# Optimization experiments

Hardware: AMD Instinct MI355X
Metric: run time of the kernel (lower is better)

The kernel has to match this reference:

```python
import jax, jax.numpy as jnp
import numpy as np

B = 8192
D_IN, D1, D2, D3, D_OUT = 784, 256, 1024, 256, 10
N_STEPS = 20
LR_INFER = 0.1
GAMMA = 0.1


def setup_inputs() -> dict:
    key = jax.random.key(0)
    ks = jax.random.split(key, 17)
    inp = {
        "x": jax.random.normal(ks[0], (B, D_IN), dtype=jnp.float32),
        # state inits (original does randn*0.1 inside forward)
        "x1_0": jax.random.normal(ks[1], (B, D1), dtype=jnp.float32) * 0.1,
        "x2_0": jax.random.normal(ks[2], (B, D2), dtype=jnp.float32) * 0.1,
        "x3_0": jax.random.normal(ks[3], (B, D3), dtype=jnp.float32) * 0.1,
        "x4_0": jax.random.normal(ks[4], (B, D_OUT), dtype=jnp.float32) * 0.1,
        # parameters (randn*0.1 per __init__)
        "W1": jax.random.normal(ks[5], (D_IN, D1), dtype=jnp.float32) * 0.1,
        "W2": jax.random.normal(ks[6], (D1, D2), dtype=jnp.float32) * 0.1,
        "W3": jax.random.normal(ks[7], (D2, D3), dtype=jnp.float32) * 0.1,
        "W4": jax.random.normal(ks[8], (D3, D_OUT), dtype=jnp.float32) * 0.1,
        "b1": jnp.zeros((D1,), dtype=jnp.float32),
        "b2": jnp.zeros((D2,), dtype=jnp.float32),
        "b3": jnp.zeros((D3,), dtype=jnp.float32),
        "b4": jnp.zeros((D_OUT,), dtype=jnp.float32),
        "L1": jax.random.normal(ks[9], (D1, D1), dtype=jnp.float32) * 0.1,
        "L2": jax.random.normal(ks[10], (D2, D2), dtype=jnp.float32) * 0.1,
        "L3": jax.random.normal(ks[11], (D3, D3), dtype=jnp.float32) * 0.1,
    }
    return inp


def reference(x, x1_0, x2_0, x3_0, x4_0, W1, W2, W3, W4, b1, b2, b3, b4, L1, L2, L3):
    sig = jax.nn.sigmoid
    # x1_pred depends only on the (constant) input x; compute once.
    x1_pred = sig(x @ W1 + b1)  # [B, D1]

    def step(carry, _):
        x1, x2, x3 = carry
        x3_pred = sig(x2 @ W3 + b3)        # [B, D3]
        x2_pred = sig(x1 @ W2 + b2)        # [B, D2]
        x4_pred = x3 @ W4 + b4             # [B, D_OUT]
        eps4 = x4_pred - x4_0
        eps3 = x3_pred - x3
        eps2 = x2_pred - x2
        eps1 = x1_pred - x1
        x3_grad = -eps3 + eps4 @ W4.T - GAMMA * (x3 @ L3)
        x2_grad = -eps2 + eps3 @ W3.T - GAMMA * (x2 @ L2)
        x1_grad = -eps1 + eps2 @ W2.T - GAMMA * (x1 @ L1)
        return (x1 - LR_INFER * x1_grad,
                x2 - LR_INFER * x2_grad,
                x3 - LR_INFER * x3_grad), None

    (x1, x2, x3), _ = jax.lax.scan(step, (x1_0, x2_0, x3_0), None, length=N_STEPS)
    return x3 @ W4 + b4  # [B, D_OUT]
```

## Files before the change

### kernel.cpp

```cpp
#include <hip/hip_runtime.h>
#include <hip/hip_bf16.h>
#include <cstdint>
#include <cstring>


#define LRC 0.1f

typedef unsigned short u16;
typedef unsigned int u32;
typedef __attribute__((ext_vector_type(4))) float f32x4;
typedef __attribute__((ext_vector_type(8))) __bf16 bf16x8;

__device__ __forceinline__ u16 f2b(float v) {
  __hip_bfloat16 h = __float2bfloat16(v);
  union { __hip_bfloat16 h; u16 u; } c; c.h = h; return c.u;
}
__device__ __forceinline__ float b2f(u16 u) {
  union { u16 u; __hip_bfloat16 h; } c; c.u = u; return __bfloat162float(c.h);
}
__device__ __forceinline__ float sigf(float x) { return 1.0f / (1.0f + expf(-x)); }

__device__ __forceinline__ void gll16(const void* g, void* l) {
  __builtin_amdgcn_global_load_lds((const __attribute__((address_space(1))) u32*)g,
                                   (__attribute__((address_space(3))) u32*)l,
                                   16, 0, 0);
}

struct GemmDesc {
  const u16* A; const u16* Bt;
  const u16* A2; const u16* Bt2;
  const float* bias; const float* master; const float* pred; const float* aux;
  const u16* eprev;
  float* outF; u16* outB;
  int lda, ldb, lda2, ldb2, K, K2, N, tnl, nblocks, epi;
};
struct Descs { GemmDesc d[6]; int nd; };

__global__ __launch_bounds__(256) void k_gemm_multi(Descs P) {
  int bid = blockIdx.x;
  int base = 0, di = 0;
  while (di + 1 < P.nd && bid >= base + P.d[di].nblocks) { base += P.d[di].nblocks; ++di; }
  const GemmDesc& d = P.d[di];
  int t = bid - base;
  int tid = threadIdx.x;

  if (d.epi == 5) {
    int i = t * 256 + tid;
    int m = i / 10, n = i - m * 10;
    if (m < 8192) {
      const float* xr = d.master + (size_t)m * 256;
      float acc = 0.f;
      #pragma unroll 4
      for (int k = 0; k < 256; ++k) acc = fmaf(xr[k], d.pred[k * 10 + n], acc);
      d.outB[(size_t)m * 32 + n] = f2b(acc + d.bias[n] - d.aux[i]);
    }
    return;
  }

  __shared__ u16 ldsA[8192];
  __shared__ u16 ldsB[8192];

  int w = tid >> 6, l = tid & 63;
  int wm = w & 1, wn = w >> 1;
  int lrow = l & 15, kgrp = l >> 4;

  int tnl = d.tnl;
  int j = t >> 3;
  int tm = (t & 7) * (d.nblocks >> (3 + tnl)) + (j >> tnl);
  int tnn = j & ((1 << tnl) - 1);
  int m0 = tm * 128, n0 = tnn * 128;

  f32x4 zero = {0.f, 0.f, 0.f, 0.f};
  f32x4 acc[4][4];
  #pragma unroll
  for (int a = 0; a < 4; ++a)
    #pragma unroll
    for (int b = 0; b < 4; ++b) acc[a][b] = zero;

  int srow = l >> 2;
  int scol = (l & 3) * 8;

  auto run = [&](const u16* A, int lda, const u16* Bt, int ldb, int K) {
    for (int k0 = 0; k0 < K;) {
      int nsub = (K - k0 >= 64) ? 2 : 1;
      for (int i = 0; i < 2 * nsub; ++i) {
        int c = i * 4 + w;
        int ks = c >> 3, rb = c & 7;
        int row = rb * 16 + srow;
        int col = k0 + ks * 32 + scol;
        gll16(A  + (size_t)(m0 + row) * lda + col, &ldsA[c * 512]);
        gll16(Bt + (size_t)(n0 + row) * ldb + col, &ldsB[c * 512]);
      }
      __syncthreads();
      for (int ks = 0; ks < nsub; ++ks) {
        bf16x8 af[4], bfr[4];
        #pragma unroll
        for (int mi = 0; mi < 4; ++mi)
          af[mi] = *(const bf16x8*)&ldsA[ks * 4096 + (wm * 64 + mi * 16 + lrow) * 32 + kgrp * 8];
        #pragma unroll
        for (int ni = 0; ni < 4; ++ni)
          bfr[ni] = *(const bf16x8*)&ldsB[ks * 4096 + (wn * 64 + ni * 16 + lrow) * 32 + kgrp * 8];
        #pragma unroll
        for (int mi = 0; mi < 4; ++mi)
          #pragma unroll
          for (int ni = 0; ni < 4; ++ni)
            acc[mi][ni] = __builtin_amdgcn_mfma_f32_16x16x32_bf16(af[mi], bfr[ni], acc[mi][ni], 0, 0, 0);
      }
      __syncthreads();
      k0 += nsub * 32;
    }
  };

  run(d.A, d.lda, d.Bt, d.ldb, d.K);
  if (d.K2 > 0) run(d.A2, d.lda2, d.Bt2, d.ldb2, d.K2);

  int epi = d.epi;
  #pragma unroll
  for (int mi = 0; mi < 4; ++mi) {
    #pragma unroll
    for (int ni = 0; ni < 4; ++ni) {
      #pragma unroll
      for (int j2 = 0; j2 < 4; ++j2) {
        int row = m0 + wm * 64 + mi * 16 + kgrp * 4 + j2;
        int col = n0 + wn * 64 + ni * 16 + lrow;
        size_t idx = (size_t)row * d.N + col;
        float a = acc[mi][ni][j2];
        if (epi == 1) {
          float s = sigf(a + d.bias[col]);
          d.outB[idx] = f2b(s - d.master[idx]);
        } else if (epi == 2) {
          d.outF[idx] = sigf(a + d.bias[col]);
        } else if (epi == 3) {
          float v = d.outF[idx];
          float nv = v + LRC * (d.pred[idx] - v) - LRC * a;
          d.outF[idx] = nv; d.outB[idx] = f2b(nv);
        } else {
          float v = d.outF[idx];
          float nv = v + LRC * b2f(d.eprev[idx]) - LRC * a;
          d.outF[idx] = nv; d.outB[idx] = f2b(nv);
        }
      }
    }
  }
}

__global__ void k_state_init(const float* __restrict__ src, float* __restrict__ dstF,
                             u16* __restrict__ dstB, int n) {
  int i = blockIdx.x * 256 + threadIdx.x;
  if (i < n) { float v = src[i]; dstF[i] = v; dstB[i] = f2b(v); }
}
__global__ void k_transpose_scale(const float* __restrict__ src, u16* __restrict__ dst,
                                  int R, int C, float scale) {
  int i = blockIdx.x * 256 + threadIdx.x;
  if (i < R * C) { int r = i / C, c = i - r * C; dst[c * R + r] = f2b(scale * src[i]); }
}
__global__ void k_conv_bf(const float* __restrict__ src, u16* __restrict__ dst, int n) {
  int i = blockIdx.x * 256 + threadIdx.x;
  if (i < n) dst[i] = f2b(src[i]);
}
__global__ void k_w4pad(const float* __restrict__ W4, u16* __restrict__ dst) {
  int i = blockIdx.x * 256 + threadIdx.x;
  if (i < 256 * 32) { int n = i >> 5, k = i & 31; dst[i] = (k < 10) ? f2b(W4[n * 10 + k]) : (u16)0; }
}
__global__ void k_zero16(u16* __restrict__ dst, int n) {
  int i = blockIdx.x * 256 + threadIdx.x;
  if (i < n) dst[i] = 0;
}
__global__ void k_xsplit(const float* __restrict__ x, u16* __restrict__ dst) {
  int i = blockIdx.x * 256 + threadIdx.x;
  if (i < 8192 * 1600) {
    int m = i / 1600, c = i - m * 1600;
    u16 o = 0;
    if (c < 784) o = f2b(x[m * 784 + c]);
    else if (c >= 800 && c < 1584) {
      float v = x[m * 784 + (c - 800)];
      float h = b2f(f2b(v));
      o = f2b(v - h);
    }
    dst[i] = o;
  }
}
__global__ void k_w1c(const float* __restrict__ W1, u16* __restrict__ dst) {
  int i = blockIdx.x * 256 + threadIdx.x;
  if (i < 256 * 1600) {
    int n = i / 1600, c = i - n * 1600;
    u16 o = 0;
    if (c < 784) o = f2b(W1[c * 256 + n]);
    else if (c >= 800 && c < 1584) o = f2b(W1[(c - 800) * 256 + n]);
    dst[i] = o;
  }
}
__global__ void k_final(const float* __restrict__ X3, const float* __restrict__ W4,
                        const float* __restrict__ b4, float* __restrict__ out) {
  int i = blockIdx.x * 256 + threadIdx.x;
  if (i < 8192 * 10) {
    int m = i / 10, n = i - m * 10;
    const float* xr = X3 + (size_t)m * 256;
    float acc = 0.f;
    #pragma unroll 4
    for (int k = 0; k < 256; ++k) acc = fmaf(xr[k], W4[k * 10 + n], acc);
    out[i] = acc + b4[n];
  }
}

extern "C" void kernel_launch(void* const* d_in, const int* in_sizes, int n_in,
                              void* d_out, int out_size, void* d_ws, size_t ws_size,
                              hipStream_t stream) {
  const float* x    = (const float*)d_in[0];
  const float* x1_0 = (const float*)d_in[1];
  const float* x2_0 = (const float*)d_in[2];
  const float* x3_0 = (const float*)d_in[3];
  const float* x4_0 = (const float*)d_in[4];
  const float* W1 = (const float*)d_in[5];
  const float* W2 = (const float*)d_in[6];
  const float* W3 = (const float*)d_in[7];
  const float* W4 = (const float*)d_in[8];
  const float* b1 = (const float*)d_in[9];
  const float* b2 = (const float*)d_in[10];
  const float* b3 = (const float*)d_in[11];
  const float* b4 = (const float*)d_in[12];
  const float* L1 = (const float*)d_in[13];
  const float* L2 = (const float*)d_in[14];
  const float* L3 = (const float*)d_in[15];

  if (ws_size < 140558336u) return;
  char* ws = (char*)d_ws;
  float* X1f   = (float*)(ws + 0);
  float* X2f   = (float*)(ws + 8388608);
  float* X3f   = (float*)(ws + 41943040);
  u16*   X1b[2]= { (u16*)(ws + 50331648), (u16*)(ws + 54525952) };
  u16*   X2b[2]= { (u16*)(ws + 58720256), (u16*)(ws + 75497472) };
  u16*   X3b[2]= { (u16*)(ws + 92274688), (u16*)(ws + 96468992) };
  float* P1    = (float*)(ws + 100663296);
  u16*   E2    = (u16*)(ws + 109051904);
  u16*   E3    = (u16*)(ws + 125829120);
  u16*   E4    = (u16*)(ws + 130023424);
  u16*   XS    = (u16*)(ws + 109051904);
  u16*   W2t   = (u16*)(ws + 135266304);
  u16*   W3t   = (u16*)(ws + 135790592);
  u16*   L1t   = (u16*)(ws + 136314880);
  u16*   L2t   = (u16*)(ws + 136445952);
  u16*   L3t   = (u16*)(ws + 138543104);
  u16*   W2b   = (u16*)(ws + 138674176);
  u16*   W3b   = (u16*)(ws + 139198464);
  u16*   W4tp  = (u16*)(ws + 139722752);
  u16*   W1c   = (u16*)(ws + 139739136);

  dim3 blk(256);
  auto G = [](int n) { return dim3((unsigned)((n + 255) / 256)); };

  k_state_init<<<G(8192*256),  blk, 0, stream>>>(x1_0, X1f, X1b[0], 8192*256);
  k_state_init<<<G(8192*1024), blk, 0, stream>>>(x2_0, X2f, X2b[0], 8192*1024);
  k_state_init<<<G(8192*256),  blk, 0, stream>>>(x3_0, X3f, X3b[0], 8192*256);
  k_transpose_scale<<<G(256*1024),  blk, 0, stream>>>(W2, W2t, 256, 1024, 1.0f);
  k_transpose_scale<<<G(1024*256),  blk, 0, stream>>>(W3, W3t, 1024, 256, 1.0f);
  k_transpose_scale<<<G(256*256),   blk, 0, stream>>>(L1, L1t, 256, 256, -0.1f);
  k_transpose_scale<<<G(1024*1024), blk, 0, stream>>>(L2, L2t, 1024, 1024, -0.1f);
  k_transpose_scale<<<G(256*256),   blk, 0, stream>>>(L3, L3t, 256, 256, -0.1f);
  k_conv_bf<<<G(256*1024), blk, 0, stream>>>(W2, W2b, 256*1024);
  k_conv_bf<<<G(1024*256), blk, 0, stream>>>(W3, W3b, 1024*256);
  k_w4pad<<<G(256*32), blk, 0, stream>>>(W4, W4tp);
  k_xsplit<<<G(8192*1600), blk, 0, stream>>>(x, XS);
  k_w1c<<<G(256*1600), blk, 0, stream>>>(W1, W1c);

  auto mkg = [](const u16* A, const u16* Bt, int lda, int ldb, int K, int N,
                int tnl, int nb, int epi) {
    GemmDesc g; memset(&g, 0, sizeof(g));
    g.A = A; g.Bt = Bt; g.lda = lda; g.ldb = ldb; g.K = K; g.N = N;
    g.tnl = tnl; g.nblocks = nb; g.epi = epi;
    return g;
  };

  {
    Descs pp; memset(&pp, 0, sizeof(pp)); pp.nd = 1;
    pp.d[0] = mkg(XS, W1c, 1600, 1600, 1600, 256, 1, 128, 2);
    pp.d[0].bias = b1; pp.d[0].outF = P1;
    k_gemm_multi<<<dim3(128), blk, 0, stream>>>(pp);
  }
  k_zero16<<<G(8192*32), blk, 0, stream>>>(E4, 8192*32);

  for (int s = 0; s < 20; ++s) {
    int p = s & 1, q = p ^ 1;

    Descs ph1; memset(&ph1, 0, sizeof(ph1)); ph1.nd = 3;
    ph1.d[0] = mkg(X2b[p], W3t, 1024, 1024, 1024, 256, 1, 128, 1);
    ph1.d[0].bias = b3; ph1.d[0].master = X3f; ph1.d[0].outB = E3;
    ph1.d[1] = mkg(X1b[p], W2t, 256, 256, 256, 1024, 3, 512, 1);
    ph1.d[1].bias = b2; ph1.d[1].master = X2f; ph1.d[1].outB = E2;
    ph1.d[2] = mkg(nullptr, nullptr, 0, 0, 0, 0, 0, 320, 5);
    ph1.d[2].master = X3f; ph1.d[2].pred = W4; ph1.d[2].bias = b4;
    ph1.d[2].aux = x4_0; ph1.d[2].outB = E4;
    k_gemm_multi<<<dim3(960), blk, 0, stream>>>(ph1);

    Descs ph2; memset(&ph2, 0, sizeof(ph2)); ph2.nd = 3;
    ph2.d[0] = mkg(E3, W3b, 256, 256, 256, 1024, 3, 512, 4);
    ph2.d[0].A2 = X2b[p]; ph2.d[0].Bt2 = L2t; ph2.d[0].lda2 = 1024;
    ph2.d[0].ldb2 = 1024; ph2.d[0].K2 = 1024;
    ph2.d[0].eprev = E2; ph2.d[0].outF = X2f; ph2.d[0].outB = X2b[q];
    ph2.d[1] = mkg(E2, W2b, 1024, 1024, 1024, 256, 1, 128, 3);
    ph2.d[1].A2 = X1b[p]; ph2.d[1].Bt2 = L1t; ph2.d[1].lda2 = 256;
    ph2.d[1].ldb2 = 256; ph2.d[1].K2 = 256;
    ph2.d[1].pred = P1; ph2.d[1].outF = X1f; ph2.d[1].outB = X1b[q];
    ph2.d[2] = mkg(E4, W4tp, 32, 32, 32, 256, 1, 128, 4);
    ph2.d[2].A2 = X3b[p]; ph2.d[2].Bt2 = L3t; ph2.d[2].lda2 = 256;
    ph2.d[2].ldb2 = 256; ph2.d[2].K2 = 256;
    ph2.d[2].eprev = E3; ph2.d[2].outF = X3f; ph2.d[2].outB = X3b[q];
    k_gemm_multi<<<dim3(768), blk, 0, stream>>>(ph2);
  }

  k_final<<<G(81920), blk, 0, stream>>>(X3f, W4, b4, (float*)d_out);
}
```

Baseline: 2.476 ms.

## Double-buffer LDS tiles so global loads overlap MFMA compute

Replaces the load-then-compute loop, which staged 64-wide K chunks, with a double-buffered pipeline over 32-wide K tiles. Both GEMM operands (A and A2) are merged into one virtual tile sequence. The next tile's global-to-LDS loads are issued before computing on the current buffer, which hides load latency and needs one barrier per tile instead of two. The trade-off is half as much compute per barrier, and correctness depends on the single barrier ordering the buffer reuse.

Result: slower. 3.545 ms (+43.2%).

```diff
diff --git a/kernel.cpp b/kernel.cpp
--- a/kernel.cpp
+++ b/kernel.cpp
@@ -80,39 +80,49 @@
   int srow = l >> 2;
   int scol = (l & 3) * 8;
 
-  auto run = [&](const u16* A, int lda, const u16* Bt, int ldb, int K) {
-    for (int k0 = 0; k0 < K;) {
-      int nsub = (K - k0 >= 64) ? 2 : 1;
-      for (int i = 0; i < 2 * nsub; ++i) {
-        int c = i * 4 + w;
-        int ks = c >> 3, rb = c & 7;
-        int row = rb * 16 + srow;
-        int col = k0 + ks * 32 + scol;
-        gll16(A  + (size_t)(m0 + row) * lda + col, &ldsA[c * 512]);
-        gll16(Bt + (size_t)(n0 + row) * ldb + col, &ldsB[c * 512]);
-      }
-      __syncthreads();
-      for (int ks = 0; ks < nsub; ++ks) {
-        bf16x8 af[4], bfr[4];
-        #pragma unroll
-        for (int mi = 0; mi < 4; ++mi)
-          af[mi] = *(const bf16x8*)&ldsA[ks * 4096 + (wm * 64 + mi * 16 + lrow) * 32 + kgrp * 8];
-        #pragma unroll
-        for (int ni = 0; ni < 4; ++ni)
-          bfr[ni] = *(const bf16x8*)&ldsB[ks * 4096 + (wn * 64 + ni * 16 + lrow) * 32 + kgrp * 8];
-        #pragma unroll
-        for (int mi = 0; mi < 4; ++mi)
-          #pragma unroll
-          for (int ni = 0; ni < 4; ++ni)
-            acc[mi][ni] = __builtin_amdgcn_mfma_f32_16x16x32_bf16(af[mi], bfr[ni], acc[mi][ni], 0, 0, 0);
-      }
-      __syncthreads();
-      k0 += nsub * 32;
+  int T1 = d.K >> 5;
+  int T  = T1 + (d.K2 >> 5);
+
+  auto stage = [&](int vt, int buf) {
+    const u16* A; const u16* Bt; int lda, ldb, k0;
+    if (vt < T1) { A = d.A;  Bt = d.Bt;  lda = d.lda;  ldb = d.ldb;  k0 = vt << 5; }
+    else         { A = d.A2; Bt = d.Bt2; lda = d.lda2; ldb = d.ldb2; k0 = (vt - T1) << 5; }
+    int bo = buf << 12;
+    #pragma unroll
+    for (int i = 0; i < 2; ++i) {
+      int c = i * 4 + w;
+      int row = c * 16 + srow;
+      int col = k0 + scol;
+      gll16(A  + (size_t)(m0 + row) * lda + col, &ldsA[bo + c * 512]);
+      gll16(Bt + (size_t)(n0 + row) * ldb + col, &ldsB[bo + c * 512]);
     }
   };
 
-  run(d.A, d.lda, d.Bt, d.ldb, d.K);
-  if (d.K2 > 0) run(d.A2, d.lda2, d.Bt2, d.ldb2, d.K2);
+  auto compute = [&](int buf) {
+    int bo = buf << 12;
+    bf16x8 af[4], bfr[4];
+    #pragma unroll
+    for (int mi = 0; mi < 4; ++mi)
+      af[mi] = *(const bf16x8*)&ldsA[bo + (wm * 64 + mi * 16 + lrow) * 32 + kgrp * 8];
+    #pragma unroll
+    for (int ni = 0; ni < 4; ++ni)
+      bfr[ni] = *(const bf16x8*)&ldsB[bo + (wn * 64 + ni * 16 + lrow) * 32 + kgrp * 8];
+    #pragma unroll
+    for (int mi = 0; mi < 4; ++mi)
+      #pragma unroll
+      for (int ni = 0; ni < 4; ++ni)
+        acc[mi][ni] = __builtin_amdgcn_mfma_f32_16x16x32_bf16(af[mi], bfr[ni], acc[mi][ni], 0, 0, 0);
+  };
+
+  stage(0, 0);
+  __syncthreads();
+  int cur = 0;
+  for (int vt = 0; vt < T; ++vt) {
+    if (vt + 1 < T) stage(vt + 1, cur ^ 1);
+    compute(cur);
+    __syncthreads();
+    cur ^= 1;
+  }
 
   int epi = d.epi;
   #pragma unroll
```

## Shrink GEMM tiles to 64x128 with two-wave blocks to double block count

Applied to the files above, without the earlier changes.

Changes the multi-GEMM kernel from 128x128 tiles with four waves to 64x128 tiles with two waves of 128 threads. Every descriptor's block count and grid size is doubled, and the LDS load loop is rewritten for the smaller A tile. The goal is more blocks than the 256 CUs can hold, so the wave tails shrink for small grids such as the 128-block P1 GEMM and the phases of 768 or 960 blocks. The cost is lower operand reuse per block, with B tiles loaded twice as often, and more global traffic.

Measured after the change: 2.509 ms. Within noise of the previous version (+1.4%).

```diff
diff --git a/kernel.cpp b/kernel.cpp
--- a/kernel.cpp
+++ b/kernel.cpp
@@ -36,7 +36,7 @@
 };
 struct Descs { GemmDesc d[6]; int nd; };
 
-__global__ __launch_bounds__(256) void k_gemm_multi(Descs P) {
+__global__ __launch_bounds__(128) void k_gemm_multi(Descs P) {
   int bid = blockIdx.x;
   int base = 0, di = 0;
   while (di + 1 < P.nd && bid >= base + P.d[di].nblocks) { base += P.d[di].nblocks; ++di; }
@@ -45,7 +45,7 @@
   int tid = threadIdx.x;
 
   if (d.epi == 5) {
-    int i = t * 256 + tid;
+    int i = t * 128 + tid;
     int m = i / 10, n = i - m * 10;
     if (m < 8192) {
       const float* xr = d.master + (size_t)m * 256;
@@ -57,18 +57,18 @@
     return;
   }
 
-  __shared__ u16 ldsA[8192];
+  __shared__ u16 ldsA[4096];
   __shared__ u16 ldsB[8192];
 
   int w = tid >> 6, l = tid & 63;
-  int wm = w & 1, wn = w >> 1;
+  int wn = w;
   int lrow = l & 15, kgrp = l >> 4;
 
   int tnl = d.tnl;
   int j = t >> 3;
   int tm = (t & 7) * (d.nblocks >> (3 + tnl)) + (j >> tnl);
   int tnn = j & ((1 << tnl) - 1);
-  int m0 = tm * 128, n0 = tnn * 128;
+  int m0 = tm * 64, n0 = tnn * 128;
 
   f32x4 zero = {0.f, 0.f, 0.f, 0.f};
   f32x4 acc[4][4];
@@ -83,20 +83,41 @@
   auto run = [&](const u16* A, int lda, const u16* Bt, int ldb, int K) {
     for (int k0 = 0; k0 < K;) {
       int nsub = (K - k0 >= 64) ? 2 : 1;
-      for (int i = 0; i < 2 * nsub; ++i) {
-        int c = i * 4 + w;
-        int ks = c >> 3, rb = c & 7;
-        int row = rb * 16 + srow;
-        int col = k0 + ks * 32 + scol;
-        gll16(A  + (size_t)(m0 + row) * lda + col, &ldsA[c * 512]);
-        gll16(Bt + (size_t)(n0 + row) * ldb + col, &ldsB[c * 512]);
+      if (nsub == 2) {
+        #pragma unroll
+        for (int i = 0; i < 12; ++i) {
+          int c = i * 2 + w;
+          if (c < 8) {
+            int ks = c >> 2, rb = c & 3;
+            gll16(A + (size_t)(m0 + rb * 16 + srow) * lda + (k0 + ks * 32 + scol),
+                  &ldsA[ks * 2048 + rb * 512]);
+          } else {
+            int c2 = c - 8;
+            int ks = c2 >> 3, rb = c2 & 7;
+            gll16(Bt + (size_t)(n0 + rb * 16 + srow) * ldb + (k0 + ks * 32 + scol),
+                  &ldsB[ks * 4096 + rb * 512]);
+          }
+        }
+      } else {
+        #pragma unroll
+        for (int i = 0; i < 6; ++i) {
+          int c = i * 2 + w;
+          if (c < 4) {
+            gll16(A + (size_t)(m0 + c * 16 + srow) * lda + (k0 + scol),
+                  &ldsA[c * 512]);
+          } else {
+            int rb = c - 4;
+            gll16(Bt + (size_t)(n0 + rb * 16 + srow) * ldb + (k0 + scol),
+                  &ldsB[rb * 512]);
+          }
+        }
       }
       __syncthreads();
       for (int ks = 0; ks < nsub; ++ks) {
         bf16x8 af[4], bfr[4];
         #pragma unroll
         for (int mi = 0; mi < 4; ++mi)
-          af[mi] = *(const bf16x8*)&ldsA[ks * 4096 + (wm * 64 + mi * 16 + lrow) * 32 + kgrp * 8];
+          af[mi] = *(const bf16x8*)&ldsA[ks * 2048 + (mi * 16 + lrow) * 32 + kgrp * 8];
         #pragma unroll
         for (int ni = 0; ni < 4; ++ni)
           bfr[ni] = *(const bf16x8*)&ldsB[ks * 4096 + (wn * 64 + ni * 16 + lrow) * 32 + kgrp * 8];
@@ -121,7 +142,7 @@
     for (int ni = 0; ni < 4; ++ni) {
       #pragma unroll
       for (int j2 = 0; j2 < 4; ++j2) {
-        int row = m0 + wm * 64 + mi * 16 + kgrp * 4 + j2;
+        int row = m0 + mi * 16 + kgrp * 4 + j2;
         int col = n0 + wn * 64 + ni * 16 + lrow;
         size_t idx = (size_t)row * d.N + col;
         float a = acc[mi][ni][j2];
@@ -247,6 +268,7 @@
   u16*   W1c   = (u16*)(ws + 139739136);
 
   dim3 blk(256);
+  dim3 gblk(128);
   auto G = [](int n) { return dim3((unsigned)((n + 255) / 256)); };
 
   k_state_init<<<G(8192*256),  blk, 0, stream>>>(x1_0, X1f, X1b[0], 8192*256);
@@ -273,9 +295,9 @@
 
   {
     Descs pp; memset(&pp, 0, sizeof(pp)); pp.nd = 1;
-    pp.d[0] = mkg(XS, W1c, 1600, 1600, 1600, 256, 1, 128, 2);
+    pp.d[0] = mkg(XS, W1c, 1600, 1600, 1600, 256, 1, 256, 2);
     pp.d[0].bias = b1; pp.d[0].outF = P1;
-    k_gemm_multi<<<dim3(128), blk, 0, stream>>>(pp);
+    k_gemm_multi<<<dim3(256), gblk, 0, stream>>>(pp);
   }
   k_zero16<<<G(8192*32), blk, 0, stream>>>(E4, 8192*32);
 
@@ -283,29 +305,29 @@
     int p = s & 1, q = p ^ 1;
 
     Descs ph1; memset(&ph1, 0, sizeof(ph1)); ph1.nd = 3;
-    ph1.d[0] = mkg(X2b[p], W3t, 1024, 1024, 1024, 256, 1, 128, 1);
+    ph1.d[0] = mkg(X2b[p], W3t, 1024, 1024, 1024, 256, 1, 256, 1);
     ph1.d[0].bias = b3; ph1.d[0].master = X3f; ph1.d[0].outB = E3;
-    ph1.d[1] = mkg(X1b[p], W2t, 256, 256, 256, 1024, 3, 512, 1);
+    ph1.d[1] = mkg(X1b[p], W2t, 256, 256, 256, 1024, 3, 1024, 1);
     ph1.d[1].bias = b2; ph1.d[1].master = X2f; ph1.d[1].outB = E2;
-    ph1.d[2] = mkg(nullptr, nullptr, 0, 0, 0, 0, 0, 320, 5);
+    ph1.d[2] = mkg(nullptr, nullptr, 0, 0, 0, 0, 0, 640, 5);
     ph1.d[2].master = X3f; ph1.d[2].pred = W4; ph1.d[2].bias = b4;
     ph1.d[2].aux = x4_0; ph1.d[2].outB = E4;
-    k_gemm_multi<<<dim3(960), blk, 0, stream>>>(ph1);
+    k_gemm_multi<<<dim3(1920), gblk, 0, stream>>>(ph1);
 
     Descs ph2; memset(&ph2, 0, sizeof(ph2)); ph2.nd = 3;
-    ph2.d[0] = mkg(E3, W3b, 256, 256, 256, 1024, 3, 512, 4);
+    ph2.d[0] = mkg(E3, W3b, 256, 256, 256, 1024, 3, 1024, 4);
     ph2.d[0].A2 = X2b[p]; ph2.d[0].Bt2 = L2t; ph2.d[0].lda2 = 1024;
     ph2.d[0].ldb2 = 1024; ph2.d[0].K2 = 1024;
     ph2.d[0].eprev = E2; ph2.d[0].outF = X2f; ph2.d[0].outB = X2b[q];
-    ph2.d[1] = mkg(E2, W2b, 1024, 1024, 1024, 256, 1, 128, 3);
+    ph2.d[1] = mkg(E2, W2b, 1024, 1024, 1024, 256, 1, 256, 3);
     ph2.d[1].A2 = X1b[p]; ph2.d[1].Bt2 = L1t; ph2.d[1].lda2 = 256;
     ph2.d[1].ldb2 = 256; ph2.d[1].K2 = 256;
     ph2.d[1].pred = P1; ph2.d[1].outF = X1f; ph2.d[1].outB = X1b[q];
-    ph2.d[2] = mkg(E4, W4tp, 32, 32, 32, 256, 1, 128, 4);
+    ph2.d[2] = mkg(E4, W4tp, 32, 32, 32, 256, 1, 256, 4);
     ph2.d[2].A2 = X3b[p]; ph2.d[2].Bt2 = L3t; ph2.d[2].lda2 = 256;
     ph2.d[2].ldb2 = 256; ph2.d[2].K2 = 256;
     ph2.d[2].eprev = E3; ph2.d[2].outF = X3f; ph2.d[2].outB = X3b[q];
-    k_gemm_multi<<<dim3(768), blk, 0, stream>>>(ph2);
+    k_gemm_multi<<<dim3(1536), gblk, 0, stream>>>(ph2);
   }
 
   k_final<<<G(81920), blk, 0, stream>>>(X3f, W4, b4, (float*)d_out);
```

## Store bf16 GEMM operands in K-tiled 32-column panel layout for contiguous loads

Applied to the files above, without the earlier changes.

All bf16 operand buffers (states, errors, weights, input split) are now stored in a panel layout: 32-wide K slices, each holding contiguous rows. Each wave's global-to-LDS load then reads a contiguous 1 KB chunk instead of 16 strided row segments. The aim is better DRAM/L2 coalescing and simpler address math in the GEMM main loop. In exchange, the epilogues now write bf16 outputs with 64-byte-strided scattered stores, and the prep kernels write through a more complex index mapping.

Result: slower. 3.320 ms (+34.1%).

```diff
diff --git a/kernel.cpp b/kernel.cpp
--- a/kernel.cpp
+++ b/kernel.cpp
@@ -24,6 +24,10 @@
   __builtin_amdgcn_global_load_lds((const __attribute__((address_space(1))) u32*)g,
                                    (__attribute__((address_space(3))) u32*)l,
                                    16, 0, 0);
+}
+
+__device__ __forceinline__ size_t tix(int R, int row, int col) {
+  return ((size_t)(col >> 5) * R + row) * 32 + (col & 31);
 }
 
 struct GemmDesc {
@@ -32,7 +36,7 @@
   const float* bias; const float* master; const float* pred; const float* aux;
   const u16* eprev;
   float* outF; u16* outB;
-  int lda, ldb, lda2, ldb2, K, K2, N, tnl, nblocks, epi;
+  int K, K2, N, tnl, nblocks, epi;
 };
 struct Descs { GemmDesc d[6]; int nd; };
 
@@ -77,19 +81,40 @@
     #pragma unroll
     for (int b = 0; b < 4; ++b) acc[a][b] = zero;
 
-  int srow = l >> 2;
-  int scol = (l & 3) * 8;
-
-  auto run = [&](const u16* A, int lda, const u16* Bt, int ldb, int K) {
+  const size_t ra = 8192 * 32;
+  const size_t rbb = (size_t)d.N * 32;
+
+  auto run = [&](const u16* A, const u16* Bt, int K) {
     for (int k0 = 0; k0 < K;) {
       int nsub = (K - k0 >= 64) ? 2 : 1;
-      for (int i = 0; i < 2 * nsub; ++i) {
-        int c = i * 4 + w;
-        int ks = c >> 3, rb = c & 7;
-        int row = rb * 16 + srow;
-        int col = k0 + ks * 32 + scol;
-        gll16(A  + (size_t)(m0 + row) * lda + col, &ldsA[c * 512]);
-        gll16(Bt + (size_t)(n0 + row) * ldb + col, &ldsB[c * 512]);
+      int kt = k0 >> 5;
+      if (nsub == 2) {
+        #pragma unroll
+        for (int i = 0; i < 8; ++i) {
+          int c = i * 4 + w;
+          if (c < 16) {
+            int ks = c >> 3, rb = c & 7;
+            gll16(A + (size_t)(kt + ks) * ra + (size_t)(m0 + rb * 16) * 32 + (l << 3),
+                  &ldsA[ks * 4096 + rb * 512]);
+          } else {
+            int c2 = c - 16, ks = c2 >> 3, rb = c2 & 7;
+            gll16(Bt + (size_t)(kt + ks) * rbb + (size_t)(n0 + rb * 16) * 32 + (l << 3),
+                  &ldsB[ks * 4096 + rb * 512]);
+          }
+        }
+      } else {
+        #pragma unroll
+        for (int i = 0; i < 4; ++i) {
+          int c = i * 4 + w;
+          if (c < 8) {
+            gll16(A + (size_t)kt * ra + (size_t)(m0 + c * 16) * 32 + (l << 3),
+                  &ldsA[c * 512]);
+          } else {
+            int rb = c - 8;
+            gll16(Bt + (size_t)kt * rbb + (size_t)(n0 + rb * 16) * 32 + (l << 3),
+                  &ldsB[rb * 512]);
+          }
+        }
       }
       __syncthreads();
       for (int ks = 0; ks < nsub; ++ks) {
@@ -111,8 +136,8 @@
     }
   };
 
-  run(d.A, d.lda, d.Bt, d.ldb, d.K);
-  if (d.K2 > 0) run(d.A2, d.lda2, d.Bt2, d.ldb2, d.K2);
+  run(d.A, d.Bt, d.K);
+  if (d.K2 > 0) run(d.A2, d.Bt2, d.K2);
 
   int epi = d.epi;
   #pragma unroll
@@ -124,20 +149,21 @@
         int row = m0 + wm * 64 + mi * 16 + kgrp * 4 + j2;
         int col = n0 + wn * 64 + ni * 16 + lrow;
         size_t idx = (size_t)row * d.N + col;
+        size_t tb  = tix(8192, row, col);
         float a = acc[mi][ni][j2];
         if (epi == 1) {
           float s = sigf(a + d.bias[col]);
-          d.outB[idx] = f2b(s - d.master[idx]);
+          d.outB[tb] = f2b(s - d.master[idx]);
         } else if (epi == 2) {
           d.outF[idx] = sigf(a + d.bias[col]);
         } else if (epi == 3) {
           float v = d.outF[idx];
           float nv = v + LRC * (d.pred[idx] - v) - LRC * a;
-          d.outF[idx] = nv; d.outB[idx] = f2b(nv);
+          d.outF[idx] = nv; d.outB[tb] = f2b(nv);
         } else {
           float v = d.outF[idx];
-          float nv = v + LRC * b2f(d.eprev[idx]) - LRC * a;
-          d.outF[idx] = nv; d.outB[idx] = f2b(nv);
+          float nv = v + LRC * b2f(d.eprev[tb]) - LRC * a;
+          d.outF[idx] = nv; d.outB[tb] = f2b(nv);
         }
       }
     }
@@ -145,18 +171,29 @@
 }
 
 __global__ void k_state_init(const float* __restrict__ src, float* __restrict__ dstF,
-                             u16* __restrict__ dstB, int n) {
-  int i = blockIdx.x * 256 + threadIdx.x;
-  if (i < n) { float v = src[i]; dstF[i] = v; dstB[i] = f2b(v); }
+                             u16* __restrict__ dstB, int C, int n) {
+  int i = blockIdx.x * 256 + threadIdx.x;
+  if (i < n) {
+    float v = src[i]; dstF[i] = v;
+    int m = i / C, c = i - m * C;
+    dstB[((size_t)(c >> 5) * 8192 + m) * 32 + (c & 31)] = f2b(v);
+  }
 }
 __global__ void k_transpose_scale(const float* __restrict__ src, u16* __restrict__ dst,
                                   int R, int C, float scale) {
   int i = blockIdx.x * 256 + threadIdx.x;
-  if (i < R * C) { int r = i / C, c = i - r * C; dst[c * R + r] = f2b(scale * src[i]); }
-}
-__global__ void k_conv_bf(const float* __restrict__ src, u16* __restrict__ dst, int n) {
-  int i = blockIdx.x * 256 + threadIdx.x;
-  if (i < n) dst[i] = f2b(src[i]);
+  if (i < R * C) {
+    int r = i / C, c = i - r * C;
+    dst[((size_t)(r >> 5) * C + c) * 32 + (r & 31)] = f2b(scale * src[i]);
+  }
+}
+__global__ void k_conv_tiled(const float* __restrict__ src, u16* __restrict__ dst,
+                             int R, int C, int n) {
+  int i = blockIdx.x * 256 + threadIdx.x;
+  if (i < n) {
+    int r = i / C, c = i - r * C;
+    dst[((size_t)(c >> 5) * R + r) * 32 + (c & 31)] = f2b(src[i]);
+  }
 }
 __global__ void k_w4pad(const float* __restrict__ W4, u16* __restrict__ dst) {
   int i = blockIdx.x * 256 + threadIdx.x;
@@ -177,7 +214,7 @@
       float h = b2f(f2b(v));
       o = f2b(v - h);
     }
-    dst[i] = o;
+    dst[((size_t)(c >> 5) * 8192 + m) * 32 + (c & 31)] = o;
   }
 }
 __global__ void k_w1c(const float* __restrict__ W1, u16* __restrict__ dst) {
@@ -187,7 +224,7 @@
     u16 o = 0;
     if (c < 784) o = f2b(W1[c * 256 + n]);
     else if (c >= 800 && c < 1584) o = f2b(W1[(c - 800) * 256 + n]);
-    dst[i] = o;
+    dst[((size_t)(c >> 5) * 256 + n) * 32 + (c & 31)] = o;
   }
 }
 __global__ void k_final(const float* __restrict__ X3, const float* __restrict__ W4,
@@ -249,31 +286,30 @@
   dim3 blk(256);
   auto G = [](int n) { return dim3((unsigned)((n + 255) / 256)); };
 
-  k_state_init<<<G(8192*256),  blk, 0, stream>>>(x1_0, X1f, X1b[0], 8192*256);
-  k_state_init<<<G(8192*1024), blk, 0, stream>>>(x2_0, X2f, X2b[0], 8192*1024);
-  k_state_init<<<G(8192*256),  blk, 0, stream>>>(x3_0, X3f, X3b[0], 8192*256);
+  k_state_init<<<G(8192*256),  blk, 0, stream>>>(x1_0, X1f, X1b[0], 256,  8192*256);
+  k_state_init<<<G(8192*1024), blk, 0, stream>>>(x2_0, X2f, X2b[0], 1024, 8192*1024);
+  k_state_init<<<G(8192*256),  blk, 0, stream>>>(x3_0, X3f, X3b[0], 256,  8192*256);
   k_transpose_scale<<<G(256*1024),  blk, 0, stream>>>(W2, W2t, 256, 1024, 1.0f);
   k_transpose_scale<<<G(1024*256),  blk, 0, stream>>>(W3, W3t, 1024, 256, 1.0f);
   k_transpose_scale<<<G(256*256),   blk, 0, stream>>>(L1, L1t, 256, 256, -0.1f);
   k_transpose_scale<<<G(1024*1024), blk, 0, stream>>>(L2, L2t, 1024, 1024, -0.1f);
   k_transpose_scale<<<G(256*256),   blk, 0, stream>>>(L3, L3t, 256, 256, -0.1f);
-  k_conv_bf<<<G(256*1024), blk, 0, stream>>>(W2, W2b, 256*1024);
-  k_conv_bf<<<G(1024*256), blk, 0, stream>>>(W3, W3b, 1024*256);
+  k_conv_tiled<<<G(256*1024), blk, 0, stream>>>(W2, W2b, 256, 1024, 256*1024);
+  k_conv_tiled<<<G(1024*256), blk, 0, stream>>>(W3, W3b, 1024, 256, 1024*256);
   k_w4pad<<<G(256*32), blk, 0, stream>>>(W4, W4tp);
   k_xsplit<<<G(8192*1600), blk, 0, stream>>>(x, XS);
   k_w1c<<<G(256*1600), blk, 0, stream>>>(W1, W1c);
 
-  auto mkg = [](const u16* A, const u16* Bt, int lda, int ldb, int K, int N,
-                int tnl, int nb, int epi) {
+  auto mkg = [](const u16* A, const u16* Bt, int K, int N, int tnl, int nb, int epi) {
     GemmDesc g; memset(&g, 0, sizeof(g));
-    g.A = A; g.Bt = Bt; g.lda = lda; g.ldb = ldb; g.K = K; g.N = N;
+    g.A = A; g.Bt = Bt; g.K = K; g.N = N;
     g.tnl = tnl; g.nblocks = nb; g.epi = epi;
     return g;
   };
 
   {
     Descs pp; memset(&pp, 0, sizeof(pp)); pp.nd = 1;
-    pp.d[0] = mkg(XS, W1c, 1600, 1600, 1600, 256, 1, 128, 2);
+    pp.d[0] = mkg(XS, W1c, 1600, 256, 1, 128, 2);
     pp.d[0].bias = b1; pp.d[0].outF = P1;
     k_gemm_multi<<<dim3(128), blk, 0, stream>>>(pp);
   }
@@ -283,27 +319,24 @@
     int p = s & 1, q = p ^ 1;
 
     Descs ph1; memset(&ph1, 0, sizeof(ph1)); ph1.nd = 3;
-    ph1.d[0] = mkg(X2b[p], W3t, 1024, 1024, 1024, 256, 1, 128, 1);
+    ph1.d[0] = mkg(X2b[p], W3t, 1024, 256, 1, 128, 1);
     ph1.d[0].bias = b3; ph1.d[0].master = X3f; ph1.d[0].outB = E3;
-    ph1.d[1] = mkg(X1b[p], W2t, 256, 256, 256, 1024, 3, 512, 1);
+    ph1.d[1] = mkg(X1b[p], W2t, 256, 1024, 3, 512, 1);
     ph1.d[1].bias = b2; ph1.d[1].master = X2f; ph1.d[1].outB = E2;
-    ph1.d[2] = mkg(nullptr, nullptr, 0, 0, 0, 0, 0, 320, 5);
+    ph1.d[2] = mkg(nullptr, nullptr, 0, 0, 0, 320, 5);
     ph1.d[2].master = X3f; ph1.d[2].pred = W4; ph1.d[2].bias = b4;
     ph1.d[2].aux = x4_0; ph1.d[2].outB = E4;
     k_gemm_multi<<<dim3(960), blk, 0, stream>>>(ph1);
 
     Descs ph2; memset(&ph2, 0, sizeof(ph2)); ph2.nd = 3;
-    ph2.d[0] = mkg(E3, W3b, 256, 256, 256, 1024, 3, 512, 4);
-    ph2.d[0].A2 = X2b[p]; ph2.d[0].Bt2 = L2t; ph2.d[0].lda2 = 1024;
-    ph2.d[0].ldb2 = 1024; ph2.d[0].K2 = 1024;
+    ph2.d[0] = mkg(E3, W3b, 256, 1024, 3, 512, 4);
+    ph2.d[0].A2 = X2b[p]; ph2.d[0].Bt2 = L2t; ph2.d[0].K2 = 1024;
     ph2.d[0].eprev = E2; ph2.d[0].outF = X2f; ph2.d[0].outB = X2b[q];
-    ph2.d[1] = mkg(E2, W2b, 1024, 1024, 1024, 256, 1, 128, 3);
-    ph2.d[1].A2 = X1b[p]; ph2.d[1].Bt2 = L1t; ph2.d[1].lda2 = 256;
-    ph2.d[1].ldb2 = 256; ph2.d[1].K2 = 256;
+    ph2.d[1] = mkg(E2, W2b, 1024, 256, 1, 128, 3);
+    ph2.d[1].A2 = X1b[p]; ph2.d[1].Bt2 = L1t; ph2.d[1].K2 = 256;
     ph2.d[1].pred = P1; ph2.d[1].outF = X1f; ph2.d[1].outB = X1b[q];
-    ph2.d[2] = mkg(E4, W4tp, 32, 32, 32, 256, 1, 128, 4);
-    ph2.d[2].A2 = X3b[p]; ph2.d[2].Bt2 = L3t; ph2.d[2].lda2 = 256;
-    ph2.d[2].ldb2 = 256; ph2.d[2].K2 = 256;
+    ph2.d[2] = mkg(E4, W4tp, 32, 256, 1, 128, 4);
+    ph2.d[2].A2 = X3b[p]; ph2.d[2].Bt2 = L3t; ph2.d[2].K2 = 256;
     ph2.d[2].eprev = E3; ph2.d[2].outF = X3f; ph2.d[2].outB = X3b[q];
     k_gemm_multi<<<dim3(768), blk, 0, stream>>>(ph2);
   }
```
